# Performance work log

Hardware: AMD Instinct MI355X
Metric: run time of the kernel (lower is better)

## Reference

```python
import jax, jax.numpy as jnp
import numpy as np

N_NODES = 50000
N_EDGES = 1600000
IN_DIM = 1024
HID = 128
N_GRAPHS = 64


def setup_inputs() -> dict:
    key = jax.random.key(0)
    ks = jax.random.split(key, 8)
    x = jax.random.normal(ks[0], (N_NODES, IN_DIM), dtype=jnp.float32)
    edge_index = jax.random.randint(ks[1], (2, N_EDGES), 0, N_NODES, dtype=jnp.int32)
    batch = jnp.sort(jax.random.randint(ks[2], (N_NODES,), 0, N_GRAPHS, dtype=jnp.int32))
    # GATConv parameters (single head, concat irrelevant for 1 head)
    glorot = 1.0 / np.sqrt(IN_DIM)
    W = jax.random.uniform(ks[3], (IN_DIM, HID), minval=-glorot, maxval=glorot, dtype=jnp.float32)
    ga = 1.0 / np.sqrt(HID)
    att_src = jax.random.uniform(ks[4], (HID,), minval=-ga, maxval=ga, dtype=jnp.float32)
    att_dst = jax.random.uniform(ks[5], (HID,), minval=-ga, maxval=ga, dtype=jnp.float32)
    bias = jnp.zeros((HID,), dtype=jnp.float32)
    return {"x": x, "W": W, "att_src": att_src, "att_dst": att_dst, "bias": bias,
            "edge_index": edge_index, "batch": batch, "num_graphs": N_GRAPHS}


def reference(x, W, att_src, att_dst, bias, edge_index, batch, num_graphs):
    N = x.shape[0]
    h = x @ W                               # [N, HID]
    # add self-loops (GATConv default add_self_loops=True)
    loops = jnp.arange(N, dtype=edge_index.dtype)
    src = jnp.concatenate([edge_index[0], loops])   # [E+N]
    dst = jnp.concatenate([edge_index[1], loops])
    a_src = h @ att_src                     # [N]
    a_dst = h @ att_dst                     # [N]
    e = jax.nn.leaky_relu(a_src[src] + a_dst[dst], negative_slope=0.2)  # [E+N]
    # scatter-softmax over incoming edges of each destination node
    m = jax.ops.segment_max(e, dst, num_segments=N)
    p = jnp.exp(e - m[dst])
    denom = jax.ops.segment_sum(p, dst, num_segments=N)
    alpha = p / denom[dst]                  # [E+N]
    # attention-weighted aggregation
    out = jax.ops.segment_sum(alpha[:, None] * h[src], dst, num_segments=N)  # [N, HID]
    out = jax.nn.relu(out + bias)
    # global max pool over graphs in the batch
    return jax.ops.segment_max(out, batch, num_segments=num_graphs)          # [G, HID]
```

## Files before the change

kernel.cpp:

```cpp
#include <hip/hip_runtime.h>
#include <hip/hip_bf16.h>

#define N_NODES 50000
#define N_EDGES 1600000
#define IN_DIM 1024
#define HID 128
#define AGG_WAVES 6144

typedef __bf16 bf16x8 __attribute__((ext_vector_type(8)));
typedef float f32x4 __attribute__((ext_vector_type(4)));
typedef __bf16 bf16x4 __attribute__((ext_vector_type(4)));

__device__ __forceinline__ float2 bf2f(unsigned u) {
    return make_float2(__uint_as_float(u << 16), __uint_as_float(u & 0xffff0000u));
}
__device__ __forceinline__ float lrelu(float v) { return v > 0.f ? v : 0.2f * v; }

__global__ void prep_kernel(const float* __restrict__ W, __bf16* __restrict__ wt,
                            int* __restrict__ deg, float* __restrict__ out, int out_n) {
    int i = blockIdx.x * 256 + threadIdx.x;
    if (i < N_NODES) deg[i] = 0;
    if (i < out_n) out[i] = 0.0f;
    if (i < HID * IN_DIM) {
        int n = i >> 10, k = i & 1023;
        wt[i] = (__bf16)W[(size_t)k * HID + n];
    }
}

__global__ __launch_bounds__(256) void gemm_kernel(const float* __restrict__ x,
                                                   const __bf16* __restrict__ wt,
                                                   __bf16* __restrict__ h2,
                                                   const float* __restrict__ att_s,
                                                   const float* __restrict__ att_d,
                                                   float* __restrict__ o_as,
                                                   float* __restrict__ o_ad,
                                                   float* __restrict__ o_ps) {
    __shared__ __bf16 xa[2][64][40];
    __shared__ __bf16 wb[2][128][40];
    const int t = threadIdx.x;
    const int m0 = blockIdx.x * 64;
    const int wid = t >> 6, lane = t & 63;
    const int lm = lane & 15, q8 = (lane >> 4) * 8;
    const int rw0 = wid * 16;

    float4 xs_reg[2];
    uint2  ws_reg[4];

    auto stage_regs = [&](int k0) {
#pragma unroll
        for (int l = 0; l < 2; ++l) {
            int f = t + l * 256;
            int row = f >> 3, kq = f & 7;
            int gr = m0 + row;
            float4 v = make_float4(0.f, 0.f, 0.f, 0.f);
            if (gr < N_NODES)
                v = *(const float4*)(x + (size_t)gr * IN_DIM + k0 + kq * 4);
            xs_reg[l] = v;
        }
#pragma unroll
        for (int l = 0; l < 4; ++l) {
            int f = t + l * 256;
            int n = f >> 3, c = f & 7;
            ws_reg[l] = *(const uint2*)(wt + (size_t)n * IN_DIM + k0 + c * 4);
        }
    };
    auto regs_to_lds = [&](int b) {
#pragma unroll
        for (int l = 0; l < 2; ++l) {
            int f = t + l * 256;
            int row = f >> 3, kq = f & 7;
            bf16x4 v;
            v[0] = (__bf16)xs_reg[l].x; v[1] = (__bf16)xs_reg[l].y;
            v[2] = (__bf16)xs_reg[l].z; v[3] = (__bf16)xs_reg[l].w;
            *(bf16x4*)&xa[b][row][kq * 4] = v;
        }
#pragma unroll
        for (int l = 0; l < 4; ++l) {
            int f = t + l * 256;
            int n = f >> 3, c = f & 7;
            *(uint2*)&wb[b][n][c * 4] = ws_reg[l];
        }
    };

    f32x4 acc[8] = {};
    stage_regs(0);
    regs_to_lds(0);
    __syncthreads();
    for (int it = 0; it < 32; ++it) {
        const int cur = it & 1;
        if (it + 1 < 32) stage_regs((it + 1) * 32);
        bf16x8 af = *(const bf16x8*)&xa[cur][rw0 + lm][q8];
#pragma unroll
        for (int ct = 0; ct < 8; ++ct) {
            bf16x8 bfr = *(const bf16x8*)&wb[cur][ct * 16 + lm][q8];
            acc[ct] = __builtin_amdgcn_mfma_f32_16x16x32_bf16(af, bfr, acc[ct], 0, 0, 0);
        }
        if (it + 1 < 32) {
            regs_to_lds(cur ^ 1);
            __syncthreads();
        }
    }
    const int quad = lane >> 4;
    float attsf[8], attdf[8];
#pragma unroll
    for (int ct = 0; ct < 8; ++ct) {
        attsf[ct] = att_s[ct * 16 + lm];
        attdf[ct] = att_d[ct * 16 + lm];
    }
#pragma unroll
    for (int reg = 0; reg < 4; ++reg) {
        int row = m0 + rw0 + quad * 4 + reg;
        float ps = 0.f, pd = 0.f;
#pragma unroll
        for (int ct = 0; ct < 8; ++ct) {
            float v = acc[ct][reg];
            ps = fmaf(v, attsf[ct], ps);
            pd = fmaf(v, attdf[ct], pd);
        }
#pragma unroll
        for (int o = 8; o; o >>= 1) {
            ps += __shfl_xor(ps, o);
            pd += __shfl_xor(pd, o);
        }
        if (row < N_NODES) {
            if (lm == 0) {
                o_as[row] = ps; o_ad[row] = pd;
                o_ps[row] = __expf(lrelu(ps + pd));
            }
#pragma unroll
            for (int ct = 0; ct < 8; ++ct)
                h2[(size_t)row * HID + ct * 16 + lm] = (__bf16)acc[ct][reg];
        }
    }
}

__global__ void hist_kernel(const int* __restrict__ ei, int* __restrict__ deg) {
    int e = blockIdx.x * 256 + threadIdx.x;
    if (e < N_EDGES) atomicAdd(&deg[ei[N_EDGES + e]], 1);
}

__global__ void scan1_kernel(const int* __restrict__ deg, int* __restrict__ bsum) {
    int b = blockIdx.x, t = threadIdx.x;
    int base = b * 1024 + t * 4;
    int s = 0;
#pragma unroll
    for (int j = 0; j < 4; ++j) {
        int idx = base + j;
        if (idx < N_NODES) s += deg[idx];
    }
    for (int o = 32; o; o >>= 1) s += __shfl_xor(s, o);
    __shared__ int wsum[4];
    int lane = t & 63, w = t >> 6;
    if (lane == 0) wsum[w] = s;
    __syncthreads();
    if (t == 0) bsum[b] = wsum[0] + wsum[1] + wsum[2] + wsum[3];
}

__global__ void scan2_kernel(const int* __restrict__ bsum, int* __restrict__ boff,
                             int* __restrict__ rowstart, int nb) {
    if (threadIdx.x == 0 && blockIdx.x == 0) {
        int run = 0;
        for (int i = 0; i < nb; ++i) { boff[i] = run; run += bsum[i]; }
        rowstart[N_NODES] = run;
    }
}

__global__ void scan3_kernel(const int* __restrict__ deg, const int* __restrict__ boff,
                             int* __restrict__ rowstart, int* __restrict__ cursor) {
    int b = blockIdx.x, t = threadIdx.x;
    int base = b * 1024 + t * 4;
    int v[4]; int s = 0;
#pragma unroll
    for (int j = 0; j < 4; ++j) {
        int idx = base + j;
        v[j] = (idx < N_NODES) ? deg[idx] : 0;
        s += v[j];
    }
    int lane = t & 63, w = t >> 6;
    int inc = s;
    for (int o = 1; o < 64; o <<= 1) {
        int u = __shfl_up(inc, o);
        if (lane >= o) inc += u;
    }
    __shared__ int wt[4];
    if (lane == 63) wt[w] = inc;
    __syncthreads();
    int woff = 0;
    for (int i = 0; i < w; ++i) woff += wt[i];
    int run = woff + inc - s + boff[b];
#pragma unroll
    for (int j = 0; j < 4; ++j) {
        int idx = base + j;
        if (idx < N_NODES) {
            rowstart[idx] = run;
            cursor[idx] = run;
            run += v[j];
        }
    }
}

__global__ void scatter_kernel(const int* __restrict__ ei, int* __restrict__ cursor,
                               uint2* __restrict__ csrp, const float* __restrict__ a_src,
                               const float* __restrict__ a_dst) {
    int e = blockIdx.x * 256 + threadIdx.x;
    if (e >= N_EDGES) return;
    int s = ei[e], d = ei[N_EDGES + e];
    int slot = atomicAdd(&cursor[d], 1);
    float pe = __expf(lrelu(a_src[s] + a_dst[d]));
    uint2 v; v.x = (unsigned)s; v.y = __float_as_uint(pe);
    csrp[slot] = v;
}

__global__ __launch_bounds__(256, 6) void aggregate_kernel(
    const uint4* __restrict__ h2q, const float* __restrict__ pself_a,
    const int* __restrict__ rowstart, const uint2* __restrict__ csrp,
    const float* __restrict__ bias, const int* __restrict__ batch,
    float* __restrict__ out) {
    const int wid = threadIdx.x >> 6, lane = threadIdx.x & 63;
    const int w = blockIdx.x * 4 + wid;
    const int quad = lane >> 4, ql = lane & 15;
    const int vq = quad << 2;
    const int q = N_NODES / AGG_WAVES;
    const int r = N_NODES - q * AGG_WAVES;
    int n0 = w * q + (w < r ? w : r);
    int n1 = n0 + q + (w < r ? 1 : 0);

    float bl[8];
    {
        const float4* b4 = (const float4*)bias;
        float4 x0 = b4[ql * 2], x1 = b4[ql * 2 + 1];
        bl[0] = x0.x; bl[1] = x0.y; bl[2] = x0.z; bl[3] = x0.w;
        bl[4] = x1.x; bl[5] = x1.y; bl[6] = x1.z; bl[7] = x1.w;
    }

    int gcur = -1;
    float m0 = 0.f, m1 = 0.f;
    for (int n = n0; n < n1; ++n) {
        int rs = rowstart[n], re = rowstart[n + 1];
        float psf = pself_a[n];
        uint4 sv = h2q[(size_t)n * 16 + ql];
        float w0 = (quad == 0) ? psf : 0.f;
        float a[8];
        {
            float2 f0 = bf2f(sv.x), f1 = bf2f(sv.y), f2 = bf2f(sv.z), f3 = bf2f(sv.w);
            a[0] = w0 * f0.x; a[1] = w0 * f0.y; a[2] = w0 * f1.x; a[3] = w0 * f1.y;
            a[4] = w0 * f2.x; a[5] = w0 * f2.y; a[6] = w0 * f3.x; a[7] = w0 * f3.y;
        }
        float pws = 0.f;
        for (int base = rs; base < re; base += 64) {
            int cnt = re - base; if (cnt > 64) cnt = 64;
            uint2 sp = make_uint2(0u, 0u);
            if (base + lane < re) sp = csrp[base + lane];
            int ngrp = (cnt + 3) >> 2;
            ngrp = (ngrp + 3) & ~3;
            for (int g = 0; g < ngrp; g += 4) {
                uint4 uu[4]; float pw[4];
#pragma unroll
                for (int i = 0; i < 4; ++i) {
                    int bidx = ((g + i) << 4) + vq;
                    unsigned bs = (unsigned)__builtin_amdgcn_ds_bpermute(bidx, (int)sp.x);
                    unsigned bp = (unsigned)__builtin_amdgcn_ds_bpermute(bidx, (int)sp.y);
                    pw[i] = __uint_as_float(bp);
                    uu[i] = h2q[bs * 16u + (unsigned)ql];
                }
#pragma unroll
                for (int i = 0; i < 4; ++i) {
                    float2 f0 = bf2f(uu[i].x), f1 = bf2f(uu[i].y);
                    float2 f2 = bf2f(uu[i].z), f3 = bf2f(uu[i].w);
                    float p = pw[i];
                    a[0] = fmaf(p, f0.x, a[0]); a[1] = fmaf(p, f0.y, a[1]);
                    a[2] = fmaf(p, f1.x, a[2]); a[3] = fmaf(p, f1.y, a[3]);
                    a[4] = fmaf(p, f2.x, a[4]); a[5] = fmaf(p, f2.y, a[5]);
                    a[6] = fmaf(p, f3.x, a[6]); a[7] = fmaf(p, f3.y, a[7]);
                    pws += p;
                }
            }
        }
#pragma unroll
        for (int k = 0; k < 8; ++k) {
            a[k] += __shfl_xor(a[k], 16);
            a[k] += __shfl_xor(a[k], 32);
        }
        pws += __shfl_xor(pws, 16);
        pws += __shfl_xor(pws, 32);
        float inv = 1.0f / (psf + pws);
        float o[8];
#pragma unroll
        for (int k = 0; k < 8; ++k) o[k] = fmaxf(fmaf(a[k], inv, bl[k]), 0.f);
        float s0 = quad == 0 ? o[0] : quad == 1 ? o[2] : quad == 2 ? o[4] : o[6];
        float s1 = quad == 0 ? o[1] : quad == 1 ? o[3] : quad == 2 ? o[5] : o[7];
        int g = batch[n];
        if (g != gcur) {
            if (gcur >= 0) {
                unsigned* outp = (unsigned*)(out + (size_t)gcur * HID);
                atomicMax(&outp[ql * 8 + 2 * quad],     __float_as_uint(m0));
                atomicMax(&outp[ql * 8 + 2 * quad + 1], __float_as_uint(m1));
            }
            gcur = g; m0 = s0; m1 = s1;
        } else {
            m0 = fmaxf(m0, s0); m1 = fmaxf(m1, s1);
        }
    }
    if (gcur >= 0) {
        unsigned* outp = (unsigned*)(out + (size_t)gcur * HID);
        atomicMax(&outp[ql * 8 + 2 * quad],     __float_as_uint(m0));
        atomicMax(&outp[ql * 8 + 2 * quad + 1], __float_as_uint(m1));
    }
}

extern "C" void kernel_launch(void* const* d_in, const int* in_sizes, int n_in,
                              void* d_out, int out_size, void* d_ws, size_t ws_size,
                              hipStream_t stream) {
    const float* x     = (const float*)d_in[0];
    const float* W     = (const float*)d_in[1];
    const float* att_s = (const float*)d_in[2];
    const float* att_d = (const float*)d_in[3];
    const float* bias  = (const float*)d_in[4];
    const int*   ei    = (const int*)d_in[5];
    const int*   batch = (const int*)d_in[6];
    float*       out   = (float*)d_out;

    char* ws = (char*)d_ws;
    size_t off = 0;
    auto alloc = [&](size_t bytes) -> void* {
        void* p = ws + off;
        off += (bytes + 255) & ~(size_t)255;
        return p;
    };
    const int NB = (N_NODES + 1023) / 1024;
    __bf16* h2       = (__bf16*)alloc((size_t)N_NODES * HID * 2);
    __bf16* wt       = (__bf16*)alloc((size_t)HID * IN_DIM * 2);
    float*  a_src    = (float*)alloc((size_t)N_NODES * 4);
    float*  a_dst    = (float*)alloc((size_t)N_NODES * 4);
    float*  pself    = (float*)alloc((size_t)N_NODES * 4);
    int*    deg      = (int*)alloc((size_t)N_NODES * 4);
    int*    rowstart = (int*)alloc((size_t)(N_NODES + 1) * 4);
    int*    cursor   = (int*)alloc((size_t)N_NODES * 4);
    int*    bsum     = (int*)alloc((size_t)NB * 4);
    int*    boff     = (int*)alloc((size_t)NB * 4);
    uint2*  csrp     = (uint2*)alloc((size_t)N_EDGES * 8);
    (void)ws_size; (void)in_sizes; (void)n_in;

    hipLaunchKernelGGL(prep_kernel, dim3(512), dim3(256), 0, stream,
                       W, wt, deg, out, out_size);
    hipLaunchKernelGGL(gemm_kernel, dim3((N_NODES + 63) / 64), dim3(256), 0, stream,
                       x, wt, h2, att_s, att_d, a_src, a_dst, pself);
    hipLaunchKernelGGL(hist_kernel, dim3((N_EDGES + 255) / 256), dim3(256), 0, stream,
                       ei, deg);
    hipLaunchKernelGGL(scan1_kernel, dim3(NB), dim3(256), 0, stream, deg, bsum);
    hipLaunchKernelGGL(scan2_kernel, dim3(1), dim3(64), 0, stream, bsum, boff, rowstart, NB);
    hipLaunchKernelGGL(scan3_kernel, dim3(NB), dim3(256), 0, stream, deg, boff, rowstart, cursor);
    hipLaunchKernelGGL(scatter_kernel, dim3((N_EDGES + 255) / 256), dim3(256), 0, stream,
                       ei, cursor, csrp, a_src, a_dst);
    hipLaunchKernelGGL(aggregate_kernel, dim3(AGG_WAVES / 4), dim3(256), 0, stream,
                       (const uint4*)h2, pself, rowstart, csrp, bias, batch, out);
}
```

Before: 522.4 us.

## Split hidden features into XCD-pinned column slices for aggregation locality

The GEMM now writes h in four column-sliced planes of 32 bf16 features each. The aggregate kernel maps blockIdx onto XCD pairs so that each pair of XCDs gathers only one slice. The goal is to make each XCD's L2 hold a smaller working set (50000×64 bytes per slice) and raise gather hit rates. Each wave handles 4 edges per step with 16 lanes reading 4 bytes each, instead of 16-byte vector loads. This means more edge-list reads (each edge is read 4 times across slices) and narrower loads. It also relies on the assumption that blocks are dispatched round-robin to XCDs.

```diff
diff --git a/kernel.cpp b/kernel.cpp
--- a/kernel.cpp
+++ b/kernel.cpp
@@ -5,7 +5,8 @@
 #define N_EDGES 1600000
 #define IN_DIM 1024
 #define HID 128
-#define AGG_WAVES 6144
+#define AGG_BLOCKS 1536
+#define SL_WAVES 1536
 
 typedef __bf16 bf16x8 __attribute__((ext_vector_type(8)));
 typedef float f32x4 __attribute__((ext_vector_type(4)));
@@ -29,7 +30,7 @@
 
 __global__ __launch_bounds__(256) void gemm_kernel(const float* __restrict__ x,
                                                    const __bf16* __restrict__ wt,
-                                                   __bf16* __restrict__ h2,
+                                                   __bf16* __restrict__ h2s,
                                                    const float* __restrict__ att_s,
                                                    const float* __restrict__ att_d,
                                                    float* __restrict__ o_as,
@@ -129,7 +130,8 @@
             }
 #pragma unroll
             for (int ct = 0; ct < 8; ++ct)
-                h2[(size_t)row * HID + ct * 16 + lm] = (__bf16)acc[ct][reg];
+                h2s[((size_t)(ct >> 1) * N_NODES + row) * 32 + (ct & 1) * 16 + lm] =
+                    (__bf16)acc[ct][reg];
         }
     }
 }
@@ -212,99 +214,73 @@
 }
 
 __global__ __launch_bounds__(256, 6) void aggregate_kernel(
-    const uint4* __restrict__ h2q, const float* __restrict__ pself_a,
+    const unsigned* __restrict__ h2s, const float* __restrict__ pself_a,
     const int* __restrict__ rowstart, const uint2* __restrict__ csrp,
     const float* __restrict__ bias, const int* __restrict__ batch,
     float* __restrict__ out) {
     const int wid = threadIdx.x >> 6, lane = threadIdx.x & 63;
-    const int w = blockIdx.x * 4 + wid;
     const int quad = lane >> 4, ql = lane & 15;
-    const int vq = quad << 2;
-    const int q = N_NODES / AGG_WAVES;
-    const int r = N_NODES - q * AGG_WAVES;
+    const int bid = blockIdx.x;
+    const int xcd = bid & 7;
+    const int slice = xcd >> 1;
+    const int sub = ((bid >> 3) << 1) | (xcd & 1);
+    const int w = sub * 4 + wid;
+    const unsigned* __restrict__ hs = h2s + (size_t)slice * N_NODES * 16;
+    const int q = N_NODES / SL_WAVES;
+    const int r = N_NODES - q * SL_WAVES;
     int n0 = w * q + (w < r ? w : r);
     int n1 = n0 + q + (w < r ? 1 : 0);
-
-    float bl[8];
-    {
-        const float4* b4 = (const float4*)bias;
-        float4 x0 = b4[ql * 2], x1 = b4[ql * 2 + 1];
-        bl[0] = x0.x; bl[1] = x0.y; bl[2] = x0.z; bl[3] = x0.w;
-        bl[4] = x1.x; bl[5] = x1.y; bl[6] = x1.z; bl[7] = x1.w;
-    }
+    const float2 bv = ((const float2*)bias)[slice * 16 + ql];
 
     int gcur = -1;
     float m0 = 0.f, m1 = 0.f;
     for (int n = n0; n < n1; ++n) {
         int rs = rowstart[n], re = rowstart[n + 1];
         float psf = pself_a[n];
-        uint4 sv = h2q[(size_t)n * 16 + ql];
-        float w0 = (quad == 0) ? psf : 0.f;
-        float a[8];
-        {
-            float2 f0 = bf2f(sv.x), f1 = bf2f(sv.y), f2 = bf2f(sv.z), f3 = bf2f(sv.w);
-            a[0] = w0 * f0.x; a[1] = w0 * f0.y; a[2] = w0 * f1.x; a[3] = w0 * f1.y;
-            a[4] = w0 * f2.x; a[5] = w0 * f2.y; a[6] = w0 * f3.x; a[7] = w0 * f3.y;
-        }
-        float pws = 0.f;
-        for (int base = rs; base < re; base += 64) {
-            int cnt = re - base; if (cnt > 64) cnt = 64;
-            uint2 sp = make_uint2(0u, 0u);
-            if (base + lane < re) sp = csrp[base + lane];
-            int ngrp = (cnt + 3) >> 2;
-            ngrp = (ngrp + 3) & ~3;
-            for (int g = 0; g < ngrp; g += 4) {
-                uint4 uu[4]; float pw[4];
-#pragma unroll
-                for (int i = 0; i < 4; ++i) {
-                    int bidx = ((g + i) << 4) + vq;
-                    unsigned bs = (unsigned)__builtin_amdgcn_ds_bpermute(bidx, (int)sp.x);
-                    unsigned bp = (unsigned)__builtin_amdgcn_ds_bpermute(bidx, (int)sp.y);
-                    pw[i] = __uint_as_float(bp);
-                    uu[i] = h2q[bs * 16u + (unsigned)ql];
-                }
-#pragma unroll
-                for (int i = 0; i < 4; ++i) {
-                    float2 f0 = bf2f(uu[i].x), f1 = bf2f(uu[i].y);
-                    float2 f2 = bf2f(uu[i].z), f3 = bf2f(uu[i].w);
-                    float p = pw[i];
-                    a[0] = fmaf(p, f0.x, a[0]); a[1] = fmaf(p, f0.y, a[1]);
-                    a[2] = fmaf(p, f1.x, a[2]); a[3] = fmaf(p, f1.y, a[3]);
-                    a[4] = fmaf(p, f2.x, a[4]); a[5] = fmaf(p, f2.y, a[5]);
-                    a[6] = fmaf(p, f3.x, a[6]); a[7] = fmaf(p, f3.y, a[7]);
-                    pws += p;
-                }
+        float a0 = 0.f, a1 = 0.f, pws = 0.f;
+        for (int e0 = rs; e0 < re; e0 += 32) {
+            unsigned uu[8]; float pw[8];
+#pragma unroll
+            for (int i = 0; i < 8; ++i) {
+                int idx = e0 + (i << 2) + quad;
+                uint2 e = make_uint2(0u, 0u);
+                if (idx < re) e = csrp[idx];
+                pw[i] = __uint_as_float(e.y);
+                uu[i] = hs[(size_t)e.x * 16 + ql];
             }
-        }
-#pragma unroll
-        for (int k = 0; k < 8; ++k) {
-            a[k] += __shfl_xor(a[k], 16);
-            a[k] += __shfl_xor(a[k], 32);
-        }
-        pws += __shfl_xor(pws, 16);
-        pws += __shfl_xor(pws, 32);
+#pragma unroll
+            for (int i = 0; i < 8; ++i) {
+                float2 f = bf2f(uu[i]);
+                a0 = fmaf(pw[i], f.x, a0);
+                a1 = fmaf(pw[i], f.y, a1);
+                pws += pw[i];
+            }
+        }
+        a0 += __shfl_xor(a0, 16); a0 += __shfl_xor(a0, 32);
+        a1 += __shfl_xor(a1, 16); a1 += __shfl_xor(a1, 32);
+        pws += __shfl_xor(pws, 16); pws += __shfl_xor(pws, 32);
+        float2 hv = bf2f(hs[(size_t)n * 16 + ql]);
+        a0 = fmaf(psf, hv.x, a0);
+        a1 = fmaf(psf, hv.y, a1);
         float inv = 1.0f / (psf + pws);
-        float o[8];
-#pragma unroll
-        for (int k = 0; k < 8; ++k) o[k] = fmaxf(fmaf(a[k], inv, bl[k]), 0.f);
-        float s0 = quad == 0 ? o[0] : quad == 1 ? o[2] : quad == 2 ? o[4] : o[6];
-        float s1 = quad == 0 ? o[1] : quad == 1 ? o[3] : quad == 2 ? o[5] : o[7];
+        float o0 = fmaxf(fmaf(a0, inv, bv.x), 0.f);
+        float o1 = fmaxf(fmaf(a1, inv, bv.y), 0.f);
         int g = batch[n];
         if (g != gcur) {
-            if (gcur >= 0) {
-                unsigned* outp = (unsigned*)(out + (size_t)gcur * HID);
-                atomicMax(&outp[ql * 8 + 2 * quad],     __float_as_uint(m0));
-                atomicMax(&outp[ql * 8 + 2 * quad + 1], __float_as_uint(m1));
+            if (gcur >= 0 && quad == 0) {
+                unsigned* outp = (unsigned*)(out + (size_t)gcur * HID + slice * 32);
+                atomicMax(&outp[2 * ql],     __float_as_uint(m0));
+                atomicMax(&outp[2 * ql + 1], __float_as_uint(m1));
             }
-            gcur = g; m0 = s0; m1 = s1;
+            gcur = g; m0 = o0; m1 = o1;
         } else {
-            m0 = fmaxf(m0, s0); m1 = fmaxf(m1, s1);
-        }
-    }
-    if (gcur >= 0) {
-        unsigned* outp = (unsigned*)(out + (size_t)gcur * HID);
-        atomicMax(&outp[ql * 8 + 2 * quad],     __float_as_uint(m0));
-        atomicMax(&outp[ql * 8 + 2 * quad + 1], __float_as_uint(m1));
+            m0 = fmaxf(m0, o0); m1 = fmaxf(m1, o1);
+        }
+    }
+    if (gcur >= 0 && quad == 0) {
+        unsigned* outp = (unsigned*)(out + (size_t)gcur * HID + slice * 32);
+        atomicMax(&outp[2 * ql],     __float_as_uint(m0));
+        atomicMax(&outp[2 * ql + 1], __float_as_uint(m1));
     }
 }
 
@@ -352,6 +328,6 @@
     hipLaunchKernelGGL(scan3_kernel, dim3(NB), dim3(256), 0, stream, deg, boff, rowstart, cursor);
     hipLaunchKernelGGL(scatter_kernel, dim3((N_EDGES + 255) / 256), dim3(256), 0, stream,
                        ei, cursor, csrp, a_src, a_dst);
-    hipLaunchKernelGGL(aggregate_kernel, dim3(AGG_WAVES / 4), dim3(256), 0, stream,
-                       (const uint4*)h2, pself, rowstart, csrp, bias, batch, out);
-}
+    hipLaunchKernelGGL(aggregate_kernel, dim3(AGG_BLOCKS), dim3(256), 0, stream,
+                       (const unsigned*)h2, pself, rowstart, csrp, bias, batch, out);
+}
```

Measured after the change: 607.1 us. 16.2% more time.
